# Optimization experiments

Measured on AMD Instinct MI355X. Metric: run time of the kernel, lower is better.

The kernel has to match this reference:

```python
import jax, jax.numpy as jnp
import numpy as np
import math

B, N, DIN, H, DH, DV, DENC, MAXLEN = 8, 1024, 1024, 8, 128, 64, 32, 1024
EPS = 1e-5


def _make_pe():
    # sinusoidal table, stored as a learnable parameter in the torch module
    pos = np.arange(MAXLEN, dtype=np.float32)[:, None]
    div = np.exp(np.arange(0, DENC, 2, dtype=np.float32) * (-math.log(10000.0) / DENC))
    pe = np.zeros((MAXLEN, DENC), np.float32)
    pe[:, 0::2] = np.sin(pos * div)
    pe[:, 1::2] = np.cos(pos * div)
    return jnp.asarray(pe)[None]  # (1, MAXLEN, DENC)


def setup_inputs() -> dict:
    key = jax.random.key(0)
    ks = jax.random.split(key, 4)
    dq = DH * H  # = d_q = d_k = 1024
    return {
        "x": jax.random.normal(ks[0], (B, N, DIN), jnp.float32),
        "gamma": jnp.ones((1, 1, DIN), jnp.float32),
        "beta": jnp.zeros((1, 1, DIN), jnp.float32),
        "pe": _make_pe(),
        "W_pos": jax.random.normal(ks[1], (DIN + DENC, DIN), jnp.float32) * 0.02,
        "b_pos": jnp.zeros((DIN,), jnp.float32),
        "W_qkv": jax.random.normal(ks[2], (DIN, 2 * dq + DV * H), jnp.float32) * 0.02,
        "b_qkv": jnp.zeros((2 * dq + DV * H,), jnp.float32),
        "W_out": jax.random.normal(ks[3], (DV * H, DIN), jnp.float32) * 0.02,
        "b_out": jnp.zeros((DIN,), jnp.float32),
        "scale": jnp.asarray(1.414, jnp.float32),
    }


def reference(x, gamma, beta, pe, W_pos, b_pos, W_qkv, b_qkv, W_out, b_out, scale):
    Bq, Nq, _ = x.shape
    # PositionalEncoding: concat sinusoidal table, project back to d_in, residual add
    pos_in = jnp.concatenate([x, jnp.broadcast_to(pe[:, :Nq], (Bq, Nq, DENC))], axis=-1)
    h = x + (pos_in @ W_pos + b_pos)
    # FeatureNorm: normalize over the SEQUENCE dim (dim=1), biased variance
    mean = h.mean(axis=1, keepdims=True)
    var = h.var(axis=1, keepdims=True)
    hn = gamma * (h - mean) * jax.lax.rsqrt(var + EPS) + beta
    # QKV projection and head split
    qkv = hn @ W_qkv + b_qkv
    dq = DH * H
    q = qkv[..., :dq].reshape(Bq, Nq, H, DH).transpose(0, 2, 1, 3)       # (B,H,N,DH)
    k = qkv[..., dq:2 * dq].reshape(Bq, Nq, H, DH).transpose(0, 2, 1, 3)  # (B,H,N,DH)
    v = qkv[..., 2 * dq:].reshape(Bq, Nq, H, DV).transpose(0, 2, 1, 3)    # (B,H,N,DV)
    # for_twdit branch: attn = softmax(-(cdist(q,k)/scale)^2) == softmax(-||q-k||^2/scale^2)
    sq = jnp.sum(q * q, axis=-1)  # (B,H,N)
    sk = jnp.sum(k * k, axis=-1)  # (B,H,N)
    d2 = sq[..., :, None] + sk[..., None, :] - 2.0 * jnp.einsum('bhnc,bhmc->bhnm', q, k)
    d2 = jnp.maximum(d2, 0.0)  # cdist is a true (nonnegative) distance
    attn = jax.nn.softmax(-d2 / (scale * scale), axis=-1)  # (B,H,N,N)
    out = jnp.einsum('bhnm,bhmd->bhnd', attn, v)            # (B,H,N,DV)
    out = out.transpose(0, 2, 1, 3).reshape(Bq, Nq, H * DV)
    return x + (out @ W_out + b_out)
```

## Files before the change

kernel.cpp:

```cpp
#include <hip/hip_runtime.h>
#include <math.h>

typedef __bf16 bf16;
typedef __attribute__((ext_vector_type(8))) __bf16 bf16x8;
typedef __attribute__((ext_vector_type(4))) float f32x4;

#define MFMA16(a, b, c) __builtin_amdgcn_mfma_f32_16x16x32_bf16(a, b, c, 0, 0, 0)

__device__ __forceinline__ void gld_lds16(const void* g, void* l) {
  __builtin_amdgcn_global_load_lds(
      (const __attribute__((address_space(1))) unsigned int*)g,
      (__attribute__((address_space(3))) unsigned int*)l, 16, 0, 0);
}

__global__ __launch_bounds__(256) void conv_bf16_kernel(const float* __restrict__ in,
                                                        bf16* __restrict__ out) {
  int idx = blockIdx.x * 256 + threadIdx.x;
  const float4 a = ((const float4*)in)[idx * 2];
  const float4 b = ((const float4*)in)[idx * 2 + 1];
  bf16x8 o = {(bf16)a.x, (bf16)a.y, (bf16)a.z, (bf16)a.w,
              (bf16)b.x, (bf16)b.y, (bf16)b.z, (bf16)b.w};
  *(bf16x8*)(out + (size_t)idx * 8) = o;
}

__global__ __launch_bounds__(256) void transpose_to_bf16(const float* __restrict__ W,
                                                         bf16* __restrict__ WT,
                                                         int K, int N) {
  __shared__ float tile[32][33];
  const int n0 = blockIdx.x * 32, k0 = blockIdx.y * 32;
  const int tx = threadIdx.x & 31, ty = threadIdx.x >> 5;
#pragma unroll
  for (int i = 0; i < 4; ++i)
    tile[ty + 8 * i][tx] = W[(size_t)(k0 + ty + 8 * i) * N + n0 + tx];
  __syncthreads();
#pragma unroll
  for (int i = 0; i < 4; ++i)
    WT[(size_t)(n0 + ty + 8 * i) * K + k0 + tx] = (bf16)tile[tx][ty + 8 * i];
}

__global__ __launch_bounds__(256) void vtrans_kernel(const bf16* __restrict__ qkv,
                                                     bf16* __restrict__ vT) {
  __shared__ bf16 tile[32][34];
  const int b = blockIdx.z;
  const int n0 = blockIdx.x * 32, c0 = blockIdx.y * 32;
  const int tx = threadIdx.x & 31, ty = threadIdx.x >> 5;
#pragma unroll
  for (int i = 0; i < 4; ++i)
    tile[ty + 8 * i][tx] = qkv[(size_t)(b * 1024 + n0 + ty + 8 * i) * 2560 + 2048 + c0 + tx];
  __syncthreads();
#pragma unroll
  for (int i = 0; i < 4; ++i)
    vT[(size_t)(b * 512 + c0 + ty + 8 * i) * 1024 + n0 + tx] = tile[tx][ty + 8 * i];
}

__global__ __launch_bounds__(256) void pe_proj_kernel(const float* __restrict__ pe,
                                                      const float* __restrict__ W_pos,
                                                      bf16* __restrict__ out) {
  int idx = blockIdx.x * 256 + threadIdx.x;
  int n = idx >> 10, c = idx & 1023;
  float s = 0.f;
#pragma unroll
  for (int e = 0; e < 32; ++e)
    s += pe[n * 32 + e] * W_pos[(size_t)(1024 + e) * 1024 + c];
  out[idx] = (bf16)s;
}

template <int NT, int OUT_BF16>
__global__ __launch_bounds__(512) void gemm_bf16(
    const bf16* __restrict__ A, const bf16* __restrict__ BT, void* __restrict__ Cout,
    int M, int N, int K,
    const float* __restrict__ bias, const float* __restrict__ add_full,
    const bf16* __restrict__ add_mod) {
  __shared__ __align__(16) bf16 As[3][128 * 64];
  __shared__ __align__(16) bf16 Bs[3][256 * 64];
  const int tid = threadIdx.x;
  const int wave = tid >> 6, lane = tid & 63;
  const int wr = wave >> 2, wc = wave & 3;
  const int lr = lane & 15, lg = lane >> 4;

  int nwg = gridDim.x * gridDim.y;
  int bid = blockIdx.y * gridDim.x + blockIdx.x;
  int s = (bid & 7) * (nwg >> 3) + (bid >> 3);
  const int row0 = (s / gridDim.x) * 128, col0 = (s % gridDim.x) * 256;

  const int trow = tid >> 3;
  const int cbd = ((tid & 7) * 16) ^ ((trow & 7) << 4);
  const bf16* asrc = A + (size_t)(row0 + trow) * K + (cbd >> 1);
  const bf16* bsrc = BT + (size_t)(col0 + trow) * K + (cbd >> 1);
  f32x4 acc[4][4] = {};

  auto STAGE = [&](int sel, int t) {
    const int kt = t * 64;
    char* al = (char*)&As[sel][0] + tid * 16;
    char* bl = (char*)&Bs[sel][0] + tid * 16;
#pragma unroll
    for (int c = 0; c < 2; ++c)
      gld_lds16(asrc + (size_t)c * 64 * K + kt, al + c * 8192);
#pragma unroll
    for (int c = 0; c < 4; ++c)
      gld_lds16(bsrc + (size_t)c * 64 * K + kt, bl + c * 8192);
  };

  STAGE(0, 0);
  if (NT > 1) STAGE(1, 1);

#pragma unroll
  for (int t = 0; t < NT; ++t) {
    if (t + 1 < NT)
      asm volatile("s_waitcnt vmcnt(6)" ::: "memory");
    else
      asm volatile("s_waitcnt vmcnt(0)" ::: "memory");
    __builtin_amdgcn_s_barrier();
    if (t + 2 < NT) STAGE((t + 2) % 3, t + 2);
    const char* Ab = (const char*)&As[t % 3][0];
    const char* Bb = (const char*)&Bs[t % 3][0];
#pragma unroll
    for (int kc = 0; kc < 2; ++kc) {
      bf16x8 af[4], bfr[4];
#pragma unroll
      for (int mt = 0; mt < 4; ++mt) {
        int r = wr * 64 + mt * 16 + lr;
        int byte = r * 128 + (((kc * 32 + lg * 8) * 2) ^ ((r & 7) << 4));
        af[mt] = *(const bf16x8*)(Ab + byte);
      }
#pragma unroll
      for (int nt = 0; nt < 4; ++nt) {
        int c = wc * 64 + nt * 16 + lr;
        int byte = c * 128 + (((kc * 32 + lg * 8) * 2) ^ ((c & 7) << 4));
        bfr[nt] = *(const bf16x8*)(Bb + byte);
      }
      __builtin_amdgcn_s_setprio(1);
#pragma unroll
      for (int mt = 0; mt < 4; ++mt)
#pragma unroll
        for (int nt = 0; nt < 4; ++nt)
          acc[mt][nt] = MFMA16(af[mt], bfr[nt], acc[mt][nt]);
      __builtin_amdgcn_s_setprio(0);
    }
  }

#pragma unroll
  for (int mt = 0; mt < 4; ++mt) {
#pragma unroll
    for (int v = 0; v < 4; ++v) {
      int r = row0 + wr * 64 + mt * 16 + lg * 4 + v;
#pragma unroll
      for (int nt = 0; nt < 4; ++nt) {
        int c = col0 + wc * 64 + nt * 16 + lr;
        float val = acc[mt][nt][v];
        if (bias) val += bias[c];
        if (add_full) val += add_full[(size_t)r * N + c];
        if (add_mod) val += (float)add_mod[(size_t)(r & 1023) * N + c];
        if (OUT_BF16)
          ((bf16*)Cout)[(size_t)r * N + c] = (bf16)val;
        else
          ((float*)Cout)[(size_t)r * N + c] = val;
      }
    }
  }
}

__global__ __launch_bounds__(512) void featnorm_kernel(const bf16* __restrict__ h,
                                                       bf16* __restrict__ hn,
                                                       const float* __restrict__ gamma,
                                                       const float* __restrict__ beta) {
  const int b = blockIdx.x >> 4;
  const int d0 = (blockIdx.x & 15) << 6;
  const int tid = threadIdx.x;
  const int c = tid & 63, g = tid >> 6;
  const size_t base = (size_t)b * (1024 * 1024) + d0 + c;
  float s = 0.f, s2 = 0.f;
  for (int n = g * 128; n < g * 128 + 128; ++n) {
    float v = (float)h[base + (size_t)n * 1024];
    s += v; s2 += v * v;
  }
  __shared__ float rs[8][64], rs2[8][64];
  rs[g][c] = s; rs2[g][c] = s2;
  __syncthreads();
  __shared__ float smean[64], srstd[64];
  if (tid < 64) {
    float S = 0.f, S2 = 0.f;
#pragma unroll
    for (int q = 0; q < 8; ++q) { S += rs[q][tid]; S2 += rs2[q][tid]; }
    float mean = S * (1.f / 1024.f);
    float var = S2 * (1.f / 1024.f) - mean * mean;
    smean[tid] = mean;
    srstd[tid] = rsqrtf(var + 1e-5f);
  }
  __syncthreads();
  const float mean = smean[c], rstd = srstd[c];
  const float gm = gamma[d0 + c], bt = beta[d0 + c];
  for (int n = g * 128; n < g * 128 + 128; ++n) {
    size_t idx = base + (size_t)n * 1024;
    hn[idx] = (bf16)(gm * ((float)h[idx] - mean) * rstd + bt);
  }
}

__global__ __launch_bounds__(256) void sk_kernel(const bf16* __restrict__ qkv,
                                                 const float* __restrict__ scale_ptr,
                                                 float* __restrict__ skl) {
  const int tid = threadIdx.x;
  const int lr = tid & 15;
  const int task = blockIdx.x * 16 + (tid >> 4);
  const int bh = task >> 10, n = task & 1023;
  const int b = bh >> 3, h = bh & 7;
  const bf16x8 v = *(const bf16x8*)(qkv + (size_t)(b * 1024 + n) * 2560 +
                                    1024 + h * 128 + lr * 8);
  float s = 0.f;
#pragma unroll
  for (int i = 0; i < 8; ++i) { float f = (float)v[i]; s += f * f; }
#pragma unroll
  for (int off = 1; off < 16; off <<= 1) s += __shfl_xor(s, off);
  if (lr == 0) {
    float sc = scale_ptr[0];
    skl[task] = s * (1.44269504f / (sc * sc));
  }
}

__global__ __launch_bounds__(256) void attn_mfma(const bf16* __restrict__ qkv,
                                                 const bf16* __restrict__ vT,
                                                 const float* __restrict__ skl,
                                                 const float* __restrict__ scale_ptr,
                                                 bf16* __restrict__ attn_o) {
  const int swz = ((blockIdx.x & 7) << 7) + (blockIdx.x >> 3);
  const int it = swz & 15, bh = swz >> 4;
  const int b = bh >> 3, h = bh & 7;
  const int i0 = it * 64;
  const int tid = threadIdx.x, wave = tid >> 6, lane = tid & 63;
  const int lr = lane & 15, lg = lane >> 4;
  const float sc = scale_ptr[0];
  const float c2 = 2.f * 1.44269504f / (sc * sc);

  __shared__ __align__(16) bf16 Ks[2][64 * 128];
  __shared__ __align__(16) bf16 Vs[2][64 * 64];
  __shared__ __align__(16) bf16 Ps[4][16 * 64];
  __shared__ float sks[1024];

  const int trowK = tid >> 4;
  const int cbKd = ((tid & 15) * 16) ^ ((trowK & 7) << 4);
  const bf16* ksrc = qkv + (size_t)(b * 1024 + trowK) * 2560 + 1024 + h * 128 + (cbKd >> 1);
  const int trowV = tid >> 3;
  const int cbVd = ((tid & 7) * 16) ^ ((trowV & 7) << 4);
  const bf16* vsrc = vT + (size_t)(b * 512 + h * 64 + trowV) * 1024 + (cbVd >> 1);

  auto STAGE = [&](int sel, int jt) {
    const bf16* kp = ksrc + (size_t)jt * 64 * 2560;
    char* kl = (char*)&Ks[sel][0] + tid * 16;
#pragma unroll
    for (int c = 0; c < 4; ++c)
      gld_lds16(kp + (size_t)c * 16 * 2560, kl + c * 4096);
    const bf16* vp = vsrc + jt * 64;
    char* vl = (char*)&Vs[sel][0] + tid * 16;
#pragma unroll
    for (int c = 0; c < 2; ++c)
      gld_lds16(vp + c * 32 * 1024, vl + c * 4096);
  };

  {
    float4 sv = ((const float4*)(skl + (size_t)bh * 1024))[tid];
    *(float4*)&sks[tid * 4] = sv;
  }
  bf16x8 qf[4];
  {
    const bf16* qrow = qkv + (size_t)(b * 1024 + i0 + wave * 16 + lr) * 2560 + h * 128;
#pragma unroll
    for (int kc = 0; kc < 4; ++kc) qf[kc] = *(const bf16x8*)(qrow + kc * 32 + lg * 8);
  }
  __syncthreads();

  bf16x8 vones;
  {
    bf16 one_or_zero = (lr == 0) ? (bf16)1.0f : (bf16)0.0f;
#pragma unroll
    for (int i = 0; i < 8; ++i) vones[i] = one_or_zero;
  }

  f32x4 o[4] = {};
  f32x4 o_l = {};

  STAGE(0, 0);
  asm volatile("s_waitcnt vmcnt(0)" ::: "memory");
  __builtin_amdgcn_s_barrier();

#pragma unroll
  for (int jt = 0; jt < 16; ++jt) {
    const int cur = jt & 1;
    if (jt < 15) STAGE(cur ^ 1, jt + 1);

    f32x4 sacc[4] = {};
    __builtin_amdgcn_s_setprio(1);
#pragma unroll
    for (int kc = 0; kc < 4; ++kc) {
#pragma unroll
      for (int nt = 0; nt < 4; ++nt) {
        int j = nt * 16 + lr;
        int byte = j * 256 + (((kc * 32 + lg * 8) * 2) ^ ((j & 7) << 4));
        bf16x8 kf = *(const bf16x8*)((const char*)&Ks[cur][0] + byte);
        sacc[nt] = MFMA16(qf[kc], kf, sacc[nt]);
      }
    }
    __builtin_amdgcn_s_setprio(0);

#pragma unroll
    for (int nt = 0; nt < 4; ++nt) {
      float skv = sks[jt * 64 + nt * 16 + lr];
#pragma unroll
      for (int v = 0; v < 4; ++v) {
        float p = __builtin_amdgcn_exp2f(sacc[nt][v] * c2 - skv);
        int r = lg * 4 + v, c = nt * 16 + lr;
        int byte = r * 128 + ((c * 2) ^ ((r & 7) << 4));
        *(bf16*)((char*)&Ps[wave][0] + byte) = (bf16)p;
      }
    }
    bf16x8 pf[2];
#pragma unroll
    for (int kc = 0; kc < 2; ++kc) {
      int byte = lr * 128 + (((kc * 32 + lg * 8) * 2) ^ ((lr & 7) << 4));
      pf[kc] = *(const bf16x8*)((const char*)&Ps[wave][0] + byte);
    }
    __builtin_amdgcn_s_setprio(1);
#pragma unroll
    for (int kc = 0; kc < 2; ++kc) {
#pragma unroll
      for (int nt = 0; nt < 4; ++nt) {
        int d = nt * 16 + lr;
        int byte = d * 128 + (((kc * 32 + lg * 8) * 2) ^ ((d & 7) << 4));
        bf16x8 vf = *(const bf16x8*)((const char*)&Vs[cur][0] + byte);
        o[nt] = MFMA16(pf[kc], vf, o[nt]);
      }
      o_l = MFMA16(pf[kc], vones, o_l);
    }
    __builtin_amdgcn_s_setprio(0);

    asm volatile("s_waitcnt vmcnt(0)" ::: "memory");
    __builtin_amdgcn_s_barrier();
  }

#pragma unroll
  for (int v = 0; v < 4; ++v) {
    float ls = __shfl(o_l[v], lg << 4);
    float inv = 1.f / ls;
    int r = i0 + wave * 16 + lg * 4 + v;
#pragma unroll
    for (int nt = 0; nt < 4; ++nt) {
      int c = h * 64 + nt * 16 + lr;
      attn_o[(size_t)(b * 1024 + r) * 512 + c] = (bf16)(o[nt][v] * inv);
    }
  }
}

extern "C" void kernel_launch(void* const* d_in, const int* in_sizes, int n_in,
                              void* d_out, int out_size, void* d_ws, size_t ws_size,
                              hipStream_t stream) {
  const float* x     = (const float*)d_in[0];
  const float* gamma = (const float*)d_in[1];
  const float* beta  = (const float*)d_in[2];
  const float* pe    = (const float*)d_in[3];
  const float* W_pos = (const float*)d_in[4];
  const float* b_pos = (const float*)d_in[5];
  const float* W_qkv = (const float*)d_in[6];
  const float* b_qkv = (const float*)d_in[7];
  const float* W_out = (const float*)d_in[8];
  const float* b_out = (const float*)d_in[9];
  const float* scale = (const float*)d_in[10];
  float* outp = (float*)d_out;

  char* ws = (char*)d_ws;
  const size_t MB = 1 << 20;
  bf16* x_bf   = (bf16*)(ws);
  bf16* hn     = (bf16*)(ws);
  bf16* wpos_t = (bf16*)(ws + 16 * MB);
  bf16* wqkv_t = (bf16*)(ws + 18 * MB);
  bf16* wout_t = (bf16*)(ws + 23 * MB);
  bf16* pe_pj  = (bf16*)(ws + 24 * MB);
  bf16* vT     = (bf16*)(ws + 24 * MB);
  bf16* h      = (bf16*)(ws + 32 * MB);
  bf16* attn_o = (bf16*)(ws + 32 * MB);
  bf16* qkv    = (bf16*)(ws + 48 * MB);
  float* skl   = (float*)(ws + 88 * MB);

  conv_bf16_kernel<<<4096, 256, 0, stream>>>(x, x_bf);
  transpose_to_bf16<<<dim3(32, 32), 256, 0, stream>>>(W_pos, wpos_t, 1024, 1024);
  transpose_to_bf16<<<dim3(80, 32), 256, 0, stream>>>(W_qkv, wqkv_t, 1024, 2560);
  transpose_to_bf16<<<dim3(32, 16), 256, 0, stream>>>(W_out, wout_t, 512, 1024);
  pe_proj_kernel<<<4096, 256, 0, stream>>>(pe, W_pos, pe_pj);
  gemm_bf16<16, 1><<<dim3(4, 64), 512, 0, stream>>>(x_bf, wpos_t, h, 8192, 1024, 1024,
                                                    b_pos, x, pe_pj);
  featnorm_kernel<<<128, 512, 0, stream>>>(h, hn, gamma, beta);
  gemm_bf16<16, 1><<<dim3(10, 64), 512, 0, stream>>>(hn, wqkv_t, qkv, 8192, 2560, 1024,
                                                     b_qkv, nullptr, nullptr);
  sk_kernel<<<4096, 256, 0, stream>>>(qkv, scale, skl);
  vtrans_kernel<<<dim3(32, 16, 8), 256, 0, stream>>>(qkv, vT);
  attn_mfma<<<1024, 256, 0, stream>>>(qkv, vT, skl, scale, attn_o);
  gemm_bf16<8, 0><<<dim3(4, 64), 512, 0, stream>>>(attn_o, wout_t, outp, 8192, 1024, 512,
                                                   b_out, x, nullptr);
}
```

Baseline: 275.0 us.

## Merge prep kernels, fuse sk with V transpose, widen attention blocks to 512 threads

The four prep kernels (x conversion, three weight transposes, PE projection) become one launch that dispatches on block index. The sk and V-transpose kernels are merged the same way, which cuts the number of launches and the gaps between them. The attention kernel now uses 512-thread blocks covering 128 query rows, so each staged K/V tile is shared by eight waves instead of four and the load per thread shrinks. This raises LDS and register pressure per block and relies on the rest of the kernel handling the new wave count.

```diff
diff --git a/kernel.cpp b/kernel.cpp
--- a/kernel.cpp
+++ b/kernel.cpp
@@ -13,56 +13,49 @@
       (__attribute__((address_space(3))) unsigned int*)l, 16, 0, 0);
 }
 
-__global__ __launch_bounds__(256) void conv_bf16_kernel(const float* __restrict__ in,
-                                                        bf16* __restrict__ out) {
-  int idx = blockIdx.x * 256 + threadIdx.x;
-  const float4 a = ((const float4*)in)[idx * 2];
-  const float4 b = ((const float4*)in)[idx * 2 + 1];
-  bf16x8 o = {(bf16)a.x, (bf16)a.y, (bf16)a.z, (bf16)a.w,
-              (bf16)b.x, (bf16)b.y, (bf16)b.z, (bf16)b.w};
-  *(bf16x8*)(out + (size_t)idx * 8) = o;
-}
-
-__global__ __launch_bounds__(256) void transpose_to_bf16(const float* __restrict__ W,
-                                                         bf16* __restrict__ WT,
-                                                         int K, int N) {
+__global__ __launch_bounds__(256) void prep_kernel(
+    const float* __restrict__ x, const float* __restrict__ W_pos,
+    const float* __restrict__ W_qkv, const float* __restrict__ W_out,
+    const float* __restrict__ pe,
+    bf16* __restrict__ x_bf, bf16* __restrict__ wpos_t, bf16* __restrict__ wqkv_t,
+    bf16* __restrict__ wout_t, bf16* __restrict__ pe_pj) {
   __shared__ float tile[32][33];
-  const int n0 = blockIdx.x * 32, k0 = blockIdx.y * 32;
-  const int tx = threadIdx.x & 31, ty = threadIdx.x >> 5;
-#pragma unroll
-  for (int i = 0; i < 4; ++i)
-    tile[ty + 8 * i][tx] = W[(size_t)(k0 + ty + 8 * i) * N + n0 + tx];
-  __syncthreads();
-#pragma unroll
-  for (int i = 0; i < 4; ++i)
-    WT[(size_t)(n0 + ty + 8 * i) * K + k0 + tx] = (bf16)tile[tx][ty + 8 * i];
-}
-
-__global__ __launch_bounds__(256) void vtrans_kernel(const bf16* __restrict__ qkv,
-                                                     bf16* __restrict__ vT) {
-  __shared__ bf16 tile[32][34];
-  const int b = blockIdx.z;
-  const int n0 = blockIdx.x * 32, c0 = blockIdx.y * 32;
-  const int tx = threadIdx.x & 31, ty = threadIdx.x >> 5;
-#pragma unroll
-  for (int i = 0; i < 4; ++i)
-    tile[ty + 8 * i][tx] = qkv[(size_t)(b * 1024 + n0 + ty + 8 * i) * 2560 + 2048 + c0 + tx];
-  __syncthreads();
-#pragma unroll
-  for (int i = 0; i < 4; ++i)
-    vT[(size_t)(b * 512 + c0 + ty + 8 * i) * 1024 + n0 + tx] = tile[tx][ty + 8 * i];
-}
-
-__global__ __launch_bounds__(256) void pe_proj_kernel(const float* __restrict__ pe,
-                                                      const float* __restrict__ W_pos,
-                                                      bf16* __restrict__ out) {
-  int idx = blockIdx.x * 256 + threadIdx.x;
+  const int tid = threadIdx.x;
+  int blk = blockIdx.x;
+  if (blk < 4096) {
+    int idx = blk * 256 + tid;
+    const float4 a = ((const float4*)x)[idx * 2];
+    const float4 b = ((const float4*)x)[idx * 2 + 1];
+    bf16x8 o = {(bf16)a.x, (bf16)a.y, (bf16)a.z, (bf16)a.w,
+                (bf16)b.x, (bf16)b.y, (bf16)b.z, (bf16)b.w};
+    *(bf16x8*)(x_bf + (size_t)idx * 8) = o;
+    return;
+  }
+  blk -= 4096;
+  if (blk < 4096) {
+    const float* W; bf16* WT; int K, N, bx, by;
+    if (blk < 1024)      { W = W_pos; WT = wpos_t; K = 1024; N = 1024; bx = blk & 31; by = blk >> 5; }
+    else if (blk < 3584) { int b2 = blk - 1024; W = W_qkv; WT = wqkv_t; K = 1024; N = 2560; bx = b2 % 80; by = b2 / 80; }
+    else                 { int b2 = blk - 3584; W = W_out; WT = wout_t; K = 512;  N = 1024; bx = b2 & 31; by = b2 >> 5; }
+    const int n0 = bx * 32, k0 = by * 32;
+    const int tx = tid & 31, ty = tid >> 5;
+#pragma unroll
+    for (int i = 0; i < 4; ++i)
+      tile[ty + 8 * i][tx] = W[(size_t)(k0 + ty + 8 * i) * N + n0 + tx];
+    __syncthreads();
+#pragma unroll
+    for (int i = 0; i < 4; ++i)
+      WT[(size_t)(n0 + ty + 8 * i) * K + k0 + tx] = (bf16)tile[tx][ty + 8 * i];
+    return;
+  }
+  blk -= 4096;
+  int idx = blk * 256 + tid;
   int n = idx >> 10, c = idx & 1023;
   float s = 0.f;
 #pragma unroll
   for (int e = 0; e < 32; ++e)
     s += pe[n * 32 + e] * W_pos[(size_t)(1024 + e) * 1024 + c];
-  out[idx] = (bf16)s;
+  pe_pj[idx] = (bf16)s;
 }
 
 template <int NT, int OUT_BF16>
@@ -78,9 +71,9 @@
   const int wr = wave >> 2, wc = wave & 3;
   const int lr = lane & 15, lg = lane >> 4;
 
-  int nwg = gridDim.x * gridDim.y;
-  int bid = blockIdx.y * gridDim.x + blockIdx.x;
-  int s = (bid & 7) * (nwg >> 3) + (bid >> 3);
+  const int nwg = gridDim.x * gridDim.y;
+  const int bid = blockIdx.y * gridDim.x + blockIdx.x;
+  const int s = (bid & 7) * (nwg >> 3) + (bid >> 3);
   const int row0 = (s / gridDim.x) * 128, col0 = (s % gridDim.x) * 256;
 
   const int trow = tid >> 3;
@@ -102,7 +95,7 @@
   };
 
   STAGE(0, 0);
-  if (NT > 1) STAGE(1, 1);
+  STAGE(1, 1);
 
 #pragma unroll
   for (int t = 0; t < NT; ++t) {
@@ -196,36 +189,53 @@
   }
 }
 
-__global__ __launch_bounds__(256) void sk_kernel(const bf16* __restrict__ qkv,
-                                                 const float* __restrict__ scale_ptr,
-                                                 float* __restrict__ skl) {
+__global__ __launch_bounds__(256) void skvt_kernel(const bf16* __restrict__ qkv,
+                                                   const float* __restrict__ scale_ptr,
+                                                   float* __restrict__ skl,
+                                                   bf16* __restrict__ vT) {
   const int tid = threadIdx.x;
-  const int lr = tid & 15;
-  const int task = blockIdx.x * 16 + (tid >> 4);
-  const int bh = task >> 10, n = task & 1023;
+  if (blockIdx.x < 4096) {
+    const int lr = tid & 15;
+    const int task = blockIdx.x * 16 + (tid >> 4);
+    const int bh = task >> 10, n = task & 1023;
+    const int b = bh >> 3, h = bh & 7;
+    const bf16x8 v = *(const bf16x8*)(qkv + (size_t)(b * 1024 + n) * 2560 +
+                                      1024 + h * 128 + lr * 8);
+    float s = 0.f;
+#pragma unroll
+    for (int i = 0; i < 8; ++i) { float f = (float)v[i]; s += f * f; }
+#pragma unroll
+    for (int off = 1; off < 16; off <<= 1) s += __shfl_xor(s, off);
+    if (lr == 0) {
+      float sc = scale_ptr[0];
+      skl[task] = s * (1.44269504f / (sc * sc));
+    }
+    return;
+  }
+  __shared__ bf16 tile[32][34];
+  const int blk = blockIdx.x - 4096;
+  const int b = blk >> 9;
+  const int rem = blk & 511;
+  const int c0 = (rem >> 5) * 32, n0 = (rem & 31) * 32;
+  const int tx = tid & 31, ty = tid >> 5;
+#pragma unroll
+  for (int i = 0; i < 4; ++i)
+    tile[ty + 8 * i][tx] = qkv[(size_t)(b * 1024 + n0 + ty + 8 * i) * 2560 + 2048 + c0 + tx];
+  __syncthreads();
+#pragma unroll
+  for (int i = 0; i < 4; ++i)
+    vT[(size_t)(b * 512 + c0 + ty + 8 * i) * 1024 + n0 + tx] = tile[tx][ty + 8 * i];
+}
+
+__global__ __launch_bounds__(512, 4) void attn_mfma(const bf16* __restrict__ qkv,
+                                                    const bf16* __restrict__ vT,
+                                                    const float* __restrict__ skl,
+                                                    const float* __restrict__ scale_ptr,
+                                                    bf16* __restrict__ attn_o) {
+  const int swz = ((blockIdx.x & 7) << 6) + (blockIdx.x >> 3);
+  const int it = swz & 7, bh = swz >> 3;
   const int b = bh >> 3, h = bh & 7;
-  const bf16x8 v = *(const bf16x8*)(qkv + (size_t)(b * 1024 + n) * 2560 +
-                                    1024 + h * 128 + lr * 8);
-  float s = 0.f;
-#pragma unroll
-  for (int i = 0; i < 8; ++i) { float f = (float)v[i]; s += f * f; }
-#pragma unroll
-  for (int off = 1; off < 16; off <<= 1) s += __shfl_xor(s, off);
-  if (lr == 0) {
-    float sc = scale_ptr[0];
-    skl[task] = s * (1.44269504f / (sc * sc));
-  }
-}
-
-__global__ __launch_bounds__(256) void attn_mfma(const bf16* __restrict__ qkv,
-                                                 const bf16* __restrict__ vT,
-                                                 const float* __restrict__ skl,
-                                                 const float* __restrict__ scale_ptr,
-                                                 bf16* __restrict__ attn_o) {
-  const int swz = ((blockIdx.x & 7) << 7) + (blockIdx.x >> 3);
-  const int it = swz & 15, bh = swz >> 4;
-  const int b = bh >> 3, h = bh & 7;
-  const int i0 = it * 64;
+  const int i0 = it * 128;
   const int tid = threadIdx.x, wave = tid >> 6, lane = tid & 63;
   const int lr = lane & 15, lg = lane >> 4;
   const float sc = scale_ptr[0];
@@ -233,7 +243,7 @@
 
   __shared__ __align__(16) bf16 Ks[2][64 * 128];
   __shared__ __align__(16) bf16 Vs[2][64 * 64];
-  __shared__ __align__(16) bf16 Ps[4][16 * 64];
+  __shared__ __align__(16) bf16 Ps[8][16 * 64];
   __shared__ float sks[1024];
 
   const int trowK = tid >> 4;
@@ -246,19 +256,14 @@
   auto STAGE = [&](int sel, int jt) {
     const bf16* kp = ksrc + (size_t)jt * 64 * 2560;
     char* kl = (char*)&Ks[sel][0] + tid * 16;
-#pragma unroll
-    for (int c = 0; c < 4; ++c)
-      gld_lds16(kp + (size_t)c * 16 * 2560, kl + c * 4096);
-    const bf16* vp = vsrc + jt * 64;
-    char* vl = (char*)&Vs[sel][0] + tid * 16;
-#pragma unroll
-    for (int c = 0; c < 2; ++c)
-      gld_lds16(vp + c * 32 * 1024, vl + c * 4096);
+    gld_lds16(kp, kl);
+    gld_lds16(kp + (size_t)32 * 2560, kl + 8192);
+    gld_lds16(vsrc + jt * 64, (char*)&Vs[sel][0] + tid * 16);
   };
 
   {
-    float4 sv = ((const float4*)(skl + (size_t)bh * 1024))[tid];
-    *(float4*)&sks[tid * 4] = sv;
+    float2 sv = ((const float2*)(skl + (size_t)bh * 1024))[tid];
+    *(float2*)&sks[tid * 2] = sv;
   }
   bf16x8 qf[4];
   {
@@ -379,19 +384,15 @@
   bf16* qkv    = (bf16*)(ws + 48 * MB);
   float* skl   = (float*)(ws + 88 * MB);
 
-  conv_bf16_kernel<<<4096, 256, 0, stream>>>(x, x_bf);
-  transpose_to_bf16<<<dim3(32, 32), 256, 0, stream>>>(W_pos, wpos_t, 1024, 1024);
-  transpose_to_bf16<<<dim3(80, 32), 256, 0, stream>>>(W_qkv, wqkv_t, 1024, 2560);
-  transpose_to_bf16<<<dim3(32, 16), 256, 0, stream>>>(W_out, wout_t, 512, 1024);
-  pe_proj_kernel<<<4096, 256, 0, stream>>>(pe, W_pos, pe_pj);
+  prep_kernel<<<12288, 256, 0, stream>>>(x, W_pos, W_qkv, W_out, pe,
+                                         x_bf, wpos_t, wqkv_t, wout_t, pe_pj);
   gemm_bf16<16, 1><<<dim3(4, 64), 512, 0, stream>>>(x_bf, wpos_t, h, 8192, 1024, 1024,
                                                     b_pos, x, pe_pj);
   featnorm_kernel<<<128, 512, 0, stream>>>(h, hn, gamma, beta);
   gemm_bf16<16, 1><<<dim3(10, 64), 512, 0, stream>>>(hn, wqkv_t, qkv, 8192, 2560, 1024,
                                                      b_qkv, nullptr, nullptr);
-  sk_kernel<<<4096, 256, 0, stream>>>(qkv, scale, skl);
-  vtrans_kernel<<<dim3(32, 16, 8), 256, 0, stream>>>(qkv, vT);
-  attn_mfma<<<1024, 256, 0, stream>>>(qkv, vT, skl, scale, attn_o);
+  skvt_kernel<<<8192, 256, 0, stream>>>(qkv, scale, skl, vT);
+  attn_mfma<<<512, 512, 0, stream>>>(qkv, vT, skl, scale, attn_o);
   gemm_bf16<8, 0><<<dim3(4, 64), 512, 0, stream>>>(attn_o, wout_t, outp, 8192, 1024, 512,
                                                    b_out, x, nullptr);
 }
```

New measurement: 257.1 us. 6.5% less time.
